# Kernel optimization log

Hardware: AMD Instinct MI355X
Metric: run time of the kernel (lower is better)

Reference implementation:

```python
import jax, jax.numpy as jnp
import numpy as np

DIM = 512  # word_hidden_size * 2


def _linear_params(key, din, dout, scale=0.05):
    kw, kb = jax.random.split(key)
    W = jax.random.normal(kw, (din, dout), dtype=jnp.float32) * scale
    b = jax.random.normal(kb, (dout,), dtype=jnp.float32) * scale
    return W, b


def setup_inputs() -> dict:
    key = jax.random.key(0)
    ks = jax.random.split(key, 16)
    S_c, S_q, B = 256, 32, 32
    inp = {
        'context_output': jax.random.normal(ks[0], (S_c, B, DIM), dtype=jnp.float32),
        'question_output': jax.random.normal(ks[1], (S_q, B, DIM), dtype=jnp.float32),
        'question_hidden_state': jax.random.normal(ks[2], (B, DIM), dtype=jnp.float32),
        'image_output': jax.random.normal(ks[3], (S_c, B, DIM), dtype=jnp.float32),
    }
    names = ['fc1', 'fc2', 'dm', 'rm', 'qm', 'rr', 'rg', 'qg']
    for i, n in enumerate(names):
        W, b = _linear_params(ks[4 + i], DIM, DIM)
        inp['W_' + n] = W
        inp['b_' + n] = b
    W_ms, b_ms = _linear_params(ks[12], DIM, 1)
    inp['W_ms'] = W_ms
    inp['b_ms'] = b_ms
    return inp


def reference(context_output, question_output, question_hidden_state, image_output,
              W_fc1, b_fc1, W_fc2, b_fc2, W_dm, b_dm, W_rm, b_rm, W_qm, b_qm,
              W_rr, b_rr, W_rg, b_rg, W_qg, b_qg, W_ms, b_ms):
    # ctx: [B, S, D] = fc1(context) + fc2(image) after seq-first -> batch-first permute
    ctx = (jnp.einsum('sbd,de->bse', context_output, W_fc1) + b_fc1
           + jnp.einsum('sbd,de->bse', image_output, W_fc2) + b_fc2)
    # hoist loop-invariant linear_dm(ctx): same math, computed once
    ctx_dm = jnp.einsum('bsd,de->bse', ctx, W_dm) + b_dm  # [B, S, D]

    B = ctx.shape[0]
    r0 = jnp.zeros((B, DIM), dtype=ctx.dtype)

    def step(r, q_t):  # r: [B, D], q_t: [B, D]
        rm = r @ W_rm + b_rm          # [B, D]
        qm = q_t @ W_qm + b_qm        # [B, D]
        m = jnp.tanh(ctx_dm + rm[:, None, :] + qm[:, None, :])  # [B, S, D]
        logits = jnp.einsum('bsd,do->bso', m, W_ms)[..., 0] + b_ms[0]  # [B, S]
        s = jax.nn.softmax(logits, axis=1)                     # [B, S]
        r_new = jnp.einsum('bs,bsd->bd', s, ctx) + jnp.tanh(r @ W_rr + b_rr)
        return r_new, None

    r, _ = jax.lax.scan(step, r0, question_output)  # scan over question tokens

    g = (r @ W_rg + b_rg) + (question_hidden_state @ W_qg + b_qg)  # [B, D]
    return g
```

## Files before the change

### kernel.cpp

```cpp
#include <hip/hip_runtime.h>
#include <hip/hip_bf16.h>

#define DIMD 512
#define NB   32
#define NS   256
#define NT   32
#define SA_STR  66
#define SCT_STR 258
#define SR_STR  132

typedef __bf16 bf16x8 __attribute__((ext_vector_type(8)));
typedef float  f32x4  __attribute__((ext_vector_type(4)));
typedef unsigned long long u64;

__device__ __forceinline__ float tanh_fast(float x) {
    float e = __expf(2.f * x);
    return 1.f - 2.f / (e + 1.f);
}

__device__ __forceinline__ void gl_lds16(const __bf16* g, __bf16* l) {
    __builtin_amdgcn_global_load_lds((const __attribute__((address_space(1))) void*)g,
                                     (__attribute__((address_space(3))) void*)l, 16, 0, 0);
}

__device__ __forceinline__ void pub64(u64* p, float v, unsigned tag) {
    u64 pk = ((u64)__float_as_uint(v) << 32) | (u64)tag;
    __hip_atomic_store(p, pk, __ATOMIC_RELAXED, __HIP_MEMORY_SCOPE_AGENT);
}
__device__ __forceinline__ float poll64(const u64* p, unsigned tag) {
    u64 v = __hip_atomic_load(p, __ATOMIC_RELAXED, __HIP_MEMORY_SCOPE_AGENT);
    while ((unsigned)v != tag) {
        __builtin_amdgcn_s_sleep(1);
        v = __hip_atomic_load(p, __ATOMIC_RELAXED, __HIP_MEMORY_SCOPE_AGENT);
    }
    return __uint_as_float((unsigned)(v >> 32));
}

__global__ void k_prep_all(const float* __restrict__ ctxin, const float* __restrict__ img,
                           const float* __restrict__ qin,
                           const float* __restrict__ Wfc1, const float* __restrict__ Wfc2,
                           const float* __restrict__ Wdm, const float* __restrict__ Wqm,
                           const float* __restrict__ Wrm, const float* __restrict__ Wrr,
                           __bf16* __restrict__ acat, __bf16* __restrict__ qp,
                           __bf16* __restrict__ wcatT, __bf16* __restrict__ wdmT,
                           __bf16* __restrict__ wqmT, __bf16* __restrict__ wrmT,
                           __bf16* __restrict__ wrrT) {
    int row = blockIdx.x;
    if (row < 8192) {
        int b = row >> 8, s = row & 255;
        const float* c  = ctxin + ((size_t)s * NB + b) * DIMD;
        const float* im = img   + ((size_t)s * NB + b) * DIMD;
        __bf16* o = acat + (size_t)row * 1024;
        for (int d = threadIdx.x; d < DIMD; d += 256) {
            o[d]       = (__bf16)c[d];
            o[512 + d] = (__bf16)im[d];
        }
    } else if (row < 10240) {
        int idx = (row - 8192) * 256 + threadIdx.x;
        qp[idx] = (__bf16)qin[idx];
    } else {
        __shared__ float tile[32][33];
        int zz = (row - 10240) >> 8;
        int idx = (row - 10240) & 255;
        int bx = idx & 15, by = idx >> 4;
        int x = threadIdx.x & 31, y = threadIdx.x >> 5;
        const float* src = (zz == 0) ? Wfc1 : (zz == 1) ? Wfc2 : (zz == 2) ? Wdm
                         : (zz == 3) ? Wqm : (zz == 4) ? Wrm : Wrr;
        __bf16* dst; int stride, off;
        if (zz < 2) { dst = wcatT; stride = 1024; off = zz * 512; }
        else {
            dst = (zz == 2) ? wdmT : (zz == 3) ? wqmT : (zz == 4) ? wrmT : wrrT;
            stride = 512; off = 0;
        }
        int c0 = bx * 32, r0 = by * 32;
#pragma unroll
        for (int k = 0; k < 32; k += 8)
            tile[y + k][x] = src[(size_t)(r0 + y + k) * DIMD + c0 + x];
        __syncthreads();
#pragma unroll
        for (int k = 0; k < 32; k += 8)
            dst[(size_t)(c0 + y + k) * stride + off + r0 + x] = (__bf16)tile[x][y + k];
    }
}

__global__ void k_post_t(const __bf16* __restrict__ ctxb, __bf16* __restrict__ ctxT,
                         const float* __restrict__ Wrg, const float* __restrict__ Wqg,
                         __bf16* __restrict__ wrgT, __bf16* __restrict__ wqgT) {
    int z = blockIdx.z;
    int x = threadIdx.x, y = threadIdx.y;
    if (z < 32) {
        if (blockIdx.y >= 8) return;
        __shared__ __bf16 tile[32][33];
        int c0 = blockIdx.x * 32, s0 = blockIdx.y * 32;
        const __bf16* S = ctxb + (size_t)z * NS * DIMD;
        __bf16* D = ctxT + (size_t)z * DIMD * NS;
#pragma unroll
        for (int k = 0; k < 32; k += 8)
            tile[y + k][x] = S[(size_t)(s0 + y + k) * DIMD + c0 + x];
        __syncthreads();
#pragma unroll
        for (int k = 0; k < 32; k += 8)
            D[(size_t)(c0 + y + k) * NS + s0 + x] = tile[x][y + k];
    } else {
        __shared__ float tf[32][33];
        const float* src = (z == 32) ? Wrg : Wqg;
        __bf16* dst = (z == 32) ? wrgT : wqgT;
        int c0 = blockIdx.x * 32, r0 = blockIdx.y * 32;
#pragma unroll
        for (int k = 0; k < 32; k += 8)
            tf[y + k][x] = src[(size_t)(r0 + y + k) * DIMD + c0 + x];
        __syncthreads();
#pragma unroll
        for (int k = 0; k < 32; k += 8)
            dst[(size_t)(c0 + y + k) * DIMD + r0 + x] = (__bf16)tf[x][y + k];
    }
}

__global__ void k_gemm64(const __bf16* __restrict__ A, const __bf16* __restrict__ BT,
                         const float* __restrict__ bias1, const float* __restrict__ bias2,
                         void* __restrict__ out, int M, int N, int K, int out_f32) {
    __shared__ __bf16 As[64 * 64];
    __shared__ __bf16 Bs[64 * 64];
    int tid = threadIdx.x, wave = tid >> 6, lane = tid & 63;
    int wm = wave >> 1, wn = wave & 1;
    int m0 = blockIdx.x * 64, n0 = blockIdx.y * 64;
    int lr = lane & 15, lq = lane >> 4;

    f32x4 acc[2][2];
#pragma unroll
    for (int i = 0; i < 2; i++)
#pragma unroll
        for (int j = 0; j < 2; j++) acc[i][j] = (f32x4){0.f, 0.f, 0.f, 0.f};

    int g0 = (wave * 2 + 0) * 64 + lane;
    int g1 = (wave * 2 + 1) * 64 + lane;
    int r0_ = g0 >> 3, c0_ = g0 & 7;
    int r1_ = g1 >> 3, c1_ = g1 & 7;
    __bf16* la0 = As + (wave * 2 + 0) * 512;
    __bf16* la1 = As + (wave * 2 + 1) * 512;
    __bf16* lb0 = Bs + (wave * 2 + 0) * 512;
    __bf16* lb1 = Bs + (wave * 2 + 1) * 512;

    for (int kk = 0; kk < K; kk += 64) {
        gl_lds16(A  + (size_t)(m0 + r0_) * K + kk + c0_ * 8, la0);
        gl_lds16(A  + (size_t)(m0 + r1_) * K + kk + c1_ * 8, la1);
        gl_lds16(BT + (size_t)(n0 + r0_) * K + kk + c0_ * 8, lb0);
        gl_lds16(BT + (size_t)(n0 + r1_) * K + kk + c1_ * 8, lb1);
        __syncthreads();
#pragma unroll
        for (int k2 = 0; k2 < 64; k2 += 32) {
            bf16x8 af[2], bfv[2];
#pragma unroll
            for (int i = 0; i < 2; i++)
                af[i] = *(const bf16x8*)(As + (wm * 32 + i * 16 + lr) * 64 + k2 + lq * 8);
#pragma unroll
            for (int j = 0; j < 2; j++)
                bfv[j] = *(const bf16x8*)(Bs + (wn * 32 + j * 16 + lr) * 64 + k2 + lq * 8);
#pragma unroll
            for (int i = 0; i < 2; i++)
#pragma unroll
                for (int j = 0; j < 2; j++)
                    acc[i][j] = __builtin_amdgcn_mfma_f32_16x16x32_bf16(af[i], bfv[j], acc[i][j], 0, 0, 0);
        }
        __syncthreads();
    }

#pragma unroll
    for (int i = 0; i < 2; i++)
#pragma unroll
        for (int j = 0; j < 2; j++) {
            int col = n0 + wn * 32 + j * 16 + lr;
            float bs = (bias1 ? bias1[col] : 0.f) + (bias2 ? bias2[col] : 0.f);
#pragma unroll
            for (int r = 0; r < 4; r++) {
                int row = m0 + wm * 32 + i * 16 + lq * 4 + r;
                float v = acc[i][j][r] + bs;
                if (out_f32) ((float*)out)[(size_t)row * N + col] = v;
                else         ((__bf16*)out)[(size_t)row * N + col] = (__bf16)v;
            }
        }
}

__global__ __launch_bounds__(512, 2) void k_scan(
    const __bf16* __restrict__ ctxdm,
    const __bf16* __restrict__ ctxT,
    const __bf16* __restrict__ wrmT,
    const __bf16* __restrict__ wrrT,
    const float* __restrict__ qmf,
    const float* __restrict__ wms, const float* __restrict__ brm,
    const float* __restrict__ brr,
    u64* parts,
    u64* rpub,
    float* __restrict__ rbuf) {
    int bid = blockIdx.x;
    int b = bid & 31, j = bid >> 5;
    int tid = threadIdx.x, wave = tid >> 6, lane = tid & 63;
    int g = lane >> 3, i = lane & 7;

    __shared__ __bf16 sA[256 * SA_STR];
    __shared__ __bf16 sCT[64 * SCT_STR];
    __shared__ float  sQ[NT * 64];
    __shared__ float  spart[NS];
    __shared__ float  sq[512];
    __shared__ float  s4[4];
    __shared__ float  sps[8 * 68];
    __shared__ float  srm[64], sh[64];
    __shared__ float  sr4[4 * SR_STR];
    __shared__ float  smv[512];

    for (int c = tid; c < 2048; c += 512) {
        int row = c >> 3, c8 = c & 7;
        *(bf16x8*)(sA + row * SA_STR + c8 * 8) =
            *(const bf16x8*)(ctxdm + ((size_t)(b * NS + row)) * DIMD + j * 64 + c8 * 8);
    }
    for (int c = tid; c < 2048; c += 512) {
        int col = c >> 5, s8 = c & 31;
        *(bf16x8*)(sCT + col * SCT_STR + s8 * 8) =
            *(const bf16x8*)(ctxT + ((size_t)(b * DIMD) + j * 64 + col) * NS + s8 * 8);
    }
    for (int c = tid; c < NT * 64; c += 512) {
        int tt = c >> 6, e = c & 63;
        sQ[c] = qmf[((size_t)tt * NB + b) * DIMD + j * 64 + e];
    }
    int m = tid >> 8, cl = (tid >> 2) & 63, q = tid & 3;
    const __bf16* wp = (m ? wrrT : wrmT) + ((size_t)(j * 64 + cl)) * DIMD + q * 128;
    bf16x8 wreg[16];
#pragma unroll
    for (int u = 0; u < 16; u++) wreg[u] = *(const bf16x8*)(wp + u * 8);

    float wm[8];
#pragma unroll
    for (int u = 0; u < 8; u++) wm[u] = wms[j * 64 + i * 8 + u];
    if (tid < 64) {
        srm[tid] = brm[j * 64 + tid];
        sh[tid]  = tanh_fast(brr[j * 64 + tid]);
    }
    __syncthreads();

    for (int t = 0; t < NT; t++) {
        unsigned tag = (unsigned)(t + 1);
        float rq[8];
#pragma unroll
        for (int u = 0; u < 8; u++) rq[u] = srm[i * 8 + u] + sQ[t * 64 + i * 8 + u];
#pragma unroll
        for (int k = 0; k < 4; k++) {
            int s = wave * 32 + k * 8 + g;
            bf16x8 cv = *(const bf16x8*)(sA + s * SA_STR + i * 8);
            float a = 0.f;
#pragma unroll
            for (int u = 0; u < 8; u++)
                a += tanh_fast((float)cv[u] + rq[u]) * wm[u];
            a += __shfl_xor(a, 1); a += __shfl_xor(a, 2); a += __shfl_xor(a, 4);
            if (i == 0) spart[s] = a;
        }
        __syncthreads();
        if (tid < NS)
            pub64(&parts[(b * 8 + j) * NS + tid], spart[tid], tag);

        {
            int s = tid >> 1, jh = (tid & 1) * 4;
            float a = 0.f;
#pragma unroll
            for (int u = 0; u < 4; u++)
                a += poll64(&parts[(b * 8 + jh + u) * NS + s], tag);
            sq[tid] = a;
        }
        __syncthreads();
        float ev = 0.f;
        if (tid < NS) { ev = __expf(sq[2 * tid] + sq[2 * tid + 1]); sq[tid] = ev; }
        else sq[tid] = 0.f;
#pragma unroll
        for (int off = 32; off; off >>= 1) ev += __shfl_xor(ev, off);
        if (tid < NS && lane == 0) s4[wave] = ev;
        __syncthreads();
        float inv = 1.f / (s4[0] + s4[1] + s4[2] + s4[3]);
        {
            const __bf16* cp = sCT + lane * SCT_STR + wave * 32;
            const float* pp = sq + wave * 32;
            float a = 0.f;
#pragma unroll
            for (int k = 0; k < 32; k += 8) {
                bf16x8 v = *(const bf16x8*)(cp + k);
#pragma unroll
                for (int u = 0; u < 8; u++) a = fmaf(pp[k + u], (float)v[u], a);
            }
            sps[wave * 68 + lane] = a;
        }
        __syncthreads();
        if (tid < 64) {
            float a = 0.f;
#pragma unroll
            for (int w2 = 0; w2 < 8; w2++) a += sps[w2 * 68 + tid];
            float rv = a * inv + sh[tid];
            if (t == NT - 1) rbuf[b * DIMD + j * 64 + tid] = rv;
            else             pub64(&rpub[b * DIMD + j * 64 + tid], rv, tag);
        }
        if (t == NT - 1) break;

        sr4[(tid >> 7) * SR_STR + (tid & 127)] = poll64(&rpub[b * DIMD + tid], tag);
        __syncthreads();
        {
            const float* sv = sr4 + q * SR_STR;
            float a0 = 0.f, a1 = 0.f;
#pragma unroll
            for (int u = 0; u < 16; u += 2) {
                bf16x8 w0 = wreg[u], w1 = wreg[u + 1];
#pragma unroll
                for (int e = 0; e < 8; e++) {
                    a0 = fmaf(sv[u * 8 + e],     (float)w0[e], a0);
                    a1 = fmaf(sv[u * 8 + 8 + e], (float)w1[e], a1);
                }
            }
            smv[tid] = a0 + a1;
        }
        __syncthreads();
        if (tid < 128) {
            int m2 = tid >> 6, cl3 = tid & 63;
            float a = smv[m2 * 256 + cl3 * 4] + smv[m2 * 256 + cl3 * 4 + 1]
                    + smv[m2 * 256 + cl3 * 4 + 2] + smv[m2 * 256 + cl3 * 4 + 3];
            int col = j * 64 + cl3;
            if (m2 == 0) srm[cl3] = a + brm[col];
            else         sh[cl3]  = tanh_fast(a + brr[col]);
        }
        __syncthreads();
    }
}

__global__ void k_final2(const float* __restrict__ r, const float* __restrict__ qh,
                         const __bf16* __restrict__ wrgT, const __bf16* __restrict__ wqgT,
                         const float* __restrict__ brg, const float* __restrict__ bqg,
                         float* __restrict__ out) {
    int clx = threadIdx.x & 7, b = threadIdx.x >> 3;
    int col = blockIdx.x * 8 + clx;
    const __bf16* w1 = wrgT + (size_t)col * DIMD;
    const __bf16* w2 = wqgT + (size_t)col * DIMD;
    const float* rp = r + (size_t)b * DIMD;
    const float* qp = qh + (size_t)b * DIMD;
    float acc = brg[col] + bqg[col];
#pragma unroll 4
    for (int d = 0; d < DIMD; d += 8) {
        bf16x8 a = *(const bf16x8*)(w1 + d);
        bf16x8 c = *(const bf16x8*)(w2 + d);
#pragma unroll
        for (int u = 0; u < 8; u++)
            acc += rp[d + u] * (float)a[u] + qp[d + u] * (float)c[u];
    }
    out[b * DIMD + col] = acc;
}


extern "C" void kernel_launch(void* const* d_in, const int* in_sizes, int n_in,
                              void* d_out, int out_size, void* d_ws, size_t ws_size,
                              hipStream_t stream) {
    const float* ctx_in = (const float*)d_in[0];
    const float* q_in   = (const float*)d_in[1];
    const float* qh     = (const float*)d_in[2];
    const float* img    = (const float*)d_in[3];
    const float* W_fc1  = (const float*)d_in[4];
    const float* b_fc1  = (const float*)d_in[5];
    const float* W_fc2  = (const float*)d_in[6];
    const float* b_fc2  = (const float*)d_in[7];
    const float* W_dm   = (const float*)d_in[8];
    const float* b_dm   = (const float*)d_in[9];
    const float* W_rm   = (const float*)d_in[10];
    const float* b_rm   = (const float*)d_in[11];
    const float* W_qm   = (const float*)d_in[12];
    const float* b_qm   = (const float*)d_in[13];
    const float* W_rr   = (const float*)d_in[14];
    const float* b_rr   = (const float*)d_in[15];
    const float* W_rg   = (const float*)d_in[16];
    const float* b_rg   = (const float*)d_in[17];
    const float* W_qg   = (const float*)d_in[18];
    const float* b_qg   = (const float*)d_in[19];
    const float* W_ms   = (const float*)d_in[20];

    char* w = (char*)d_ws;
    __bf16* acat  = (__bf16*)w;  w += (size_t)8192 * 1024 * 2;
    __bf16* qp    = (__bf16*)w;  w += (size_t)1024 * 512 * 2;
    __bf16* wcatT = (__bf16*)w;  w += (size_t)512 * 1024 * 2;
    __bf16* wdmT  = (__bf16*)w;  w += (size_t)512 * 512 * 2;
    __bf16* wqmT  = (__bf16*)w;  w += (size_t)512 * 512 * 2;
    __bf16* wrmT  = (__bf16*)w;  w += (size_t)512 * 512 * 2;
    __bf16* wrrT  = (__bf16*)w;  w += (size_t)512 * 512 * 2;
    __bf16* ctxb  = (__bf16*)w;  w += (size_t)8192 * 512 * 2;
    __bf16* ctxdm = (__bf16*)w;  w += (size_t)8192 * 512 * 2;
    char* x = (char*)acat;
    __bf16* ctxT  = (__bf16*)x;  x += (size_t)NB * DIMD * NS * 2;
    float*  qmf   = (float*)x;   x += (size_t)1024 * 512 * 4;
    __bf16* wrgT  = (__bf16*)x;  x += (size_t)512 * 512 * 2;
    __bf16* wqgT  = (__bf16*)x;  x += (size_t)512 * 512 * 2;
    u64*    rpub  = (u64*)x;     x += (size_t)NB * DIMD * 8;
    u64*    parts = (u64*)x;     x += (size_t)NB * 8 * NS * 8;
    float*  rbuf  = (float*)x;   x += (size_t)NB * DIMD * 4;

    k_prep_all<<<11776, 256, 0, stream>>>(ctx_in, img, q_in, W_fc1, W_fc2, W_dm,
                                          W_qm, W_rm, W_rr, acat, qp,
                                          wcatT, wdmT, wqmT, wrmT, wrrT);
    k_gemm64<<<dim3(128, 8), 256, 0, stream>>>(acat, wcatT, b_fc1, b_fc2, ctxb, 8192, 512, 1024, 0);
    k_post_t<<<dim3(16, 16, 34), dim3(32, 8), 0, stream>>>(ctxb, ctxT, W_rg, W_qg, wrgT, wqgT);
    k_gemm64<<<dim3(128, 8), 256, 0, stream>>>(ctxb, wdmT, b_dm, nullptr, ctxdm, 8192, 512, 512, 0);
    k_gemm64<<<dim3(16, 8), 256, 0, stream>>>(qp, wqmT, b_qm, nullptr, qmf, 1024, 512, 512, 1);

    k_scan<<<256, 512, 0, stream>>>(ctxdm, ctxT, wrmT, wrrT, qmf, W_ms,
                                    b_rm, b_rr, parts, rpub, rbuf);

    k_final2<<<64, 256, 0, stream>>>(rbuf, qh, wrgT, wqgT, b_rg, b_qg, (float*)d_out);
}
```

Measured before the change: 467.5 us.

## Merge post-GEMM kernels into one launch and publish scan partials without barrier

Moves the Wrg/Wqg transposes into the prep kernel and merges the ctx transpose, the ctx_dm GEMM and the qm GEMM into one heterogeneous kernel launch. This cuts three launches to one and lets the independent work run concurrently. In the scan, each lane group publishes its partial logit directly instead of staging it through shared memory behind a barrier. The consumer side polls all four partials in one loop rather than one after another. The main cost being targeted is launch and serialization overhead plus per-step sync latency in the recurrent scan, at the price of a larger, mixed-role kernel.

Result: faster. 447.7 us (-4.2%).

```diff
diff --git a/kernel.cpp b/kernel.cpp
--- a/kernel.cpp
+++ b/kernel.cpp
@@ -41,10 +41,12 @@
                            const float* __restrict__ Wfc1, const float* __restrict__ Wfc2,
                            const float* __restrict__ Wdm, const float* __restrict__ Wqm,
                            const float* __restrict__ Wrm, const float* __restrict__ Wrr,
+                           const float* __restrict__ Wrg, const float* __restrict__ Wqg,
                            __bf16* __restrict__ acat, __bf16* __restrict__ qp,
                            __bf16* __restrict__ wcatT, __bf16* __restrict__ wdmT,
                            __bf16* __restrict__ wqmT, __bf16* __restrict__ wrmT,
-                           __bf16* __restrict__ wrrT) {
+                           __bf16* __restrict__ wrrT, __bf16* __restrict__ wrgT,
+                           __bf16* __restrict__ wqgT) {
     int row = blockIdx.x;
     if (row < 8192) {
         int b = row >> 8, s = row & 255;
@@ -65,11 +67,13 @@
         int bx = idx & 15, by = idx >> 4;
         int x = threadIdx.x & 31, y = threadIdx.x >> 5;
         const float* src = (zz == 0) ? Wfc1 : (zz == 1) ? Wfc2 : (zz == 2) ? Wdm
-                         : (zz == 3) ? Wqm : (zz == 4) ? Wrm : Wrr;
+                         : (zz == 3) ? Wqm : (zz == 4) ? Wrm : (zz == 5) ? Wrr
+                         : (zz == 6) ? Wrg : Wqg;
         __bf16* dst; int stride, off;
         if (zz < 2) { dst = wcatT; stride = 1024; off = zz * 512; }
         else {
-            dst = (zz == 2) ? wdmT : (zz == 3) ? wqmT : (zz == 4) ? wrmT : wrrT;
+            dst = (zz == 2) ? wdmT : (zz == 3) ? wqmT : (zz == 4) ? wrmT
+                : (zz == 5) ? wrrT : (zz == 6) ? wrgT : wqgT;
             stride = 512; off = 0;
         }
         int c0 = bx * 32, r0 = by * 32;
@@ -83,47 +87,15 @@
     }
 }
 
-__global__ void k_post_t(const __bf16* __restrict__ ctxb, __bf16* __restrict__ ctxT,
-                         const float* __restrict__ Wrg, const float* __restrict__ Wqg,
-                         __bf16* __restrict__ wrgT, __bf16* __restrict__ wqgT) {
-    int z = blockIdx.z;
-    int x = threadIdx.x, y = threadIdx.y;
-    if (z < 32) {
-        if (blockIdx.y >= 8) return;
-        __shared__ __bf16 tile[32][33];
-        int c0 = blockIdx.x * 32, s0 = blockIdx.y * 32;
-        const __bf16* S = ctxb + (size_t)z * NS * DIMD;
-        __bf16* D = ctxT + (size_t)z * DIMD * NS;
-#pragma unroll
-        for (int k = 0; k < 32; k += 8)
-            tile[y + k][x] = S[(size_t)(s0 + y + k) * DIMD + c0 + x];
-        __syncthreads();
-#pragma unroll
-        for (int k = 0; k < 32; k += 8)
-            D[(size_t)(c0 + y + k) * NS + s0 + x] = tile[x][y + k];
-    } else {
-        __shared__ float tf[32][33];
-        const float* src = (z == 32) ? Wrg : Wqg;
-        __bf16* dst = (z == 32) ? wrgT : wqgT;
-        int c0 = blockIdx.x * 32, r0 = blockIdx.y * 32;
-#pragma unroll
-        for (int k = 0; k < 32; k += 8)
-            tf[y + k][x] = src[(size_t)(r0 + y + k) * DIMD + c0 + x];
-        __syncthreads();
-#pragma unroll
-        for (int k = 0; k < 32; k += 8)
-            dst[(size_t)(c0 + y + k) * DIMD + r0 + x] = (__bf16)tf[x][y + k];
-    }
-}
-
-__global__ void k_gemm64(const __bf16* __restrict__ A, const __bf16* __restrict__ BT,
-                         const float* __restrict__ bias1, const float* __restrict__ bias2,
-                         void* __restrict__ out, int M, int N, int K, int out_f32) {
-    __shared__ __bf16 As[64 * 64];
-    __shared__ __bf16 Bs[64 * 64];
+__device__ __forceinline__ void gemm_tile(const __bf16* __restrict__ A,
+                                          const __bf16* __restrict__ BT,
+                                          const float* __restrict__ bias1,
+                                          const float* __restrict__ bias2,
+                                          void* __restrict__ out, int N, int K,
+                                          int m0, int n0, int out_f32,
+                                          __bf16* As, __bf16* Bs) {
     int tid = threadIdx.x, wave = tid >> 6, lane = tid & 63;
     int wm = wave >> 1, wn = wave & 1;
-    int m0 = blockIdx.x * 64, n0 = blockIdx.y * 64;
     int lr = lane & 15, lq = lane >> 4;
 
     f32x4 acc[2][2];
@@ -179,6 +151,47 @@
                 else         ((__bf16*)out)[(size_t)row * N + col] = (__bf16)v;
             }
         }
+}
+
+__global__ void k_gemm64(const __bf16* __restrict__ A, const __bf16* __restrict__ BT,
+                         const float* __restrict__ bias1, const float* __restrict__ bias2,
+                         void* __restrict__ out, int M, int N, int K, int out_f32) {
+    __shared__ __bf16 As[64 * 64];
+    __shared__ __bf16 Bs[64 * 64];
+    gemm_tile(A, BT, bias1, bias2, out, N, K, blockIdx.x * 64, blockIdx.y * 64, out_f32, As, Bs);
+}
+
+__global__ void k_fused(const __bf16* __restrict__ ctxb, const __bf16* __restrict__ wdmT,
+                        const float* __restrict__ bdm, __bf16* __restrict__ ctxdm,
+                        const __bf16* __restrict__ qp, const __bf16* __restrict__ wqmT,
+                        const float* __restrict__ bqm, float* __restrict__ qmf,
+                        __bf16* __restrict__ ctxT) {
+    __shared__ __bf16 As[64 * 64];
+    __shared__ __bf16 Bs[64 * 64];
+    int bid = blockIdx.x;
+    if (bid < 1024) {
+        gemm_tile(ctxb, wdmT, bdm, nullptr, ctxdm, 512, 512,
+                  (bid & 127) * 64, (bid >> 7) * 64, 0, As, Bs);
+    } else if (bid < 1152) {
+        int b2 = bid - 1024;
+        gemm_tile(qp, wqmT, bqm, nullptr, qmf, 512, 512,
+                  (b2 & 15) * 64, (b2 >> 4) * 64, 1, As, Bs);
+    } else {
+        int b3 = bid - 1152;
+        int z = b3 >> 7, rest = b3 & 127;
+        int c0 = (rest & 15) * 32, s0 = (rest >> 4) * 32;
+        __bf16* tile = As;
+        int x = threadIdx.x & 31, y = threadIdx.x >> 5;
+        const __bf16* S = ctxb + (size_t)z * NS * DIMD;
+        __bf16* D = ctxT + (size_t)z * DIMD * NS;
+#pragma unroll
+        for (int k = 0; k < 32; k += 8)
+            tile[(y + k) * 33 + x] = S[(size_t)(s0 + y + k) * DIMD + c0 + x];
+        __syncthreads();
+#pragma unroll
+        for (int k = 0; k < 32; k += 8)
+            D[(size_t)(c0 + y + k) * NS + s0 + x] = tile[x * 33 + y + k];
+    }
 }
 
 __global__ __launch_bounds__(512, 2) void k_scan(
@@ -200,8 +213,8 @@
     __shared__ __bf16 sA[256 * SA_STR];
     __shared__ __bf16 sCT[64 * SCT_STR];
     __shared__ float  sQ[NT * 64];
-    __shared__ float  spart[NS];
     __shared__ float  sq[512];
+    __shared__ float  sp[256];
     __shared__ float  s4[4];
     __shared__ float  sps[8 * 68];
     __shared__ float  srm[64], sh[64];
@@ -251,24 +264,31 @@
             for (int u = 0; u < 8; u++)
                 a += tanh_fast((float)cv[u] + rq[u]) * wm[u];
             a += __shfl_xor(a, 1); a += __shfl_xor(a, 2); a += __shfl_xor(a, 4);
-            if (i == 0) spart[s] = a;
-        }
-        __syncthreads();
-        if (tid < NS)
-            pub64(&parts[(b * 8 + j) * NS + tid], spart[tid], tag);
+            if (i == 0) pub64(&parts[(b * 8 + j) * NS + s], a, tag);
+        }
 
         {
             int s = tid >> 1, jh = (tid & 1) * 4;
-            float a = 0.f;
-#pragma unroll
-            for (int u = 0; u < 4; u++)
-                a += poll64(&parts[(b * 8 + jh + u) * NS + s], tag);
-            sq[tid] = a;
+            const u64* p0 = &parts[(b * 8 + jh + 0) * NS + s];
+            const u64* p1 = &parts[(b * 8 + jh + 1) * NS + s];
+            const u64* p2 = &parts[(b * 8 + jh + 2) * NS + s];
+            const u64* p3 = &parts[(b * 8 + jh + 3) * NS + s];
+            u64 v0, v1, v2, v3;
+            for (;;) {
+                v0 = __hip_atomic_load(p0, __ATOMIC_RELAXED, __HIP_MEMORY_SCOPE_AGENT);
+                v1 = __hip_atomic_load(p1, __ATOMIC_RELAXED, __HIP_MEMORY_SCOPE_AGENT);
+                v2 = __hip_atomic_load(p2, __ATOMIC_RELAXED, __HIP_MEMORY_SCOPE_AGENT);
+                v3 = __hip_atomic_load(p3, __ATOMIC_RELAXED, __HIP_MEMORY_SCOPE_AGENT);
+                if ((unsigned)v0 == tag && (unsigned)v1 == tag &&
+                    (unsigned)v2 == tag && (unsigned)v3 == tag) break;
+                __builtin_amdgcn_s_sleep(1);
+            }
+            sq[tid] = __uint_as_float((unsigned)(v0 >> 32)) + __uint_as_float((unsigned)(v1 >> 32))
+                    + __uint_as_float((unsigned)(v2 >> 32)) + __uint_as_float((unsigned)(v3 >> 32));
         }
         __syncthreads();
         float ev = 0.f;
-        if (tid < NS) { ev = __expf(sq[2 * tid] + sq[2 * tid + 1]); sq[tid] = ev; }
-        else sq[tid] = 0.f;
+        if (tid < NS) { ev = __expf(sq[2 * tid] + sq[2 * tid + 1]); sp[tid] = ev; }
 #pragma unroll
         for (int off = 32; off; off >>= 1) ev += __shfl_xor(ev, off);
         if (tid < NS && lane == 0) s4[wave] = ev;
@@ -276,7 +296,7 @@
         float inv = 1.f / (s4[0] + s4[1] + s4[2] + s4[3]);
         {
             const __bf16* cp = sCT + lane * SCT_STR + wave * 32;
-            const float* pp = sq + wave * 32;
+            const float* pp = sp + wave * 32;
             float a = 0.f;
 #pragma unroll
             for (int k = 0; k < 32; k += 8) {
@@ -382,27 +402,23 @@
     __bf16* wqmT  = (__bf16*)w;  w += (size_t)512 * 512 * 2;
     __bf16* wrmT  = (__bf16*)w;  w += (size_t)512 * 512 * 2;
     __bf16* wrrT  = (__bf16*)w;  w += (size_t)512 * 512 * 2;
+    __bf16* wrgT  = (__bf16*)w;  w += (size_t)512 * 512 * 2;
+    __bf16* wqgT  = (__bf16*)w;  w += (size_t)512 * 512 * 2;
     __bf16* ctxb  = (__bf16*)w;  w += (size_t)8192 * 512 * 2;
     __bf16* ctxdm = (__bf16*)w;  w += (size_t)8192 * 512 * 2;
     char* x = (char*)acat;
     __bf16* ctxT  = (__bf16*)x;  x += (size_t)NB * DIMD * NS * 2;
     float*  qmf   = (float*)x;   x += (size_t)1024 * 512 * 4;
-    __bf16* wrgT  = (__bf16*)x;  x += (size_t)512 * 512 * 2;
-    __bf16* wqgT  = (__bf16*)x;  x += (size_t)512 * 512 * 2;
     u64*    rpub  = (u64*)x;     x += (size_t)NB * DIMD * 8;
     u64*    parts = (u64*)x;     x += (size_t)NB * 8 * NS * 8;
     float*  rbuf  = (float*)x;   x += (size_t)NB * DIMD * 4;
 
-    k_prep_all<<<11776, 256, 0, stream>>>(ctx_in, img, q_in, W_fc1, W_fc2, W_dm,
-                                          W_qm, W_rm, W_rr, acat, qp,
-                                          wcatT, wdmT, wqmT, wrmT, wrrT);
+    k_prep_all<<<12288, 256, 0, stream>>>(ctx_in, img, q_in, W_fc1, W_fc2, W_dm,
+                                          W_qm, W_rm, W_rr, W_rg, W_qg, acat, qp,
+                                          wcatT, wdmT, wqmT, wrmT, wrrT, wrgT, wqgT);
     k_gemm64<<<dim3(128, 8), 256, 0, stream>>>(acat, wcatT, b_fc1, b_fc2, ctxb, 8192, 512, 1024, 0);
-    k_post_t<<<dim3(16, 16, 34), dim3(32, 8), 0, stream>>>(ctxb, ctxT, W_rg, W_qg, wrgT, wqgT);
-    k_gemm64<<<dim3(128, 8), 256, 0, stream>>>(ctxb, wdmT, b_dm, nullptr, ctxdm, 8192, 512, 512, 0);
-    k_gemm64<<<dim3(16, 8), 256, 0, stream>>>(qp, wqmT, b_qm, nullptr, qmf, 1024, 512, 512, 1);
-
+    k_fused<<<5248, 256, 0, stream>>>(ctxb, wdmT, b_dm, ctxdm, qp, wqmT, b_qm, qmf, ctxT);
     k_scan<<<256, 512, 0, stream>>>(ctxdm, ctxT, wrmT, wrrT, qmf, W_ms,
                                     b_rm, b_rr, parts, rpub, rbuf);
-
     k_final2<<<64, 256, 0, stream>>>(rbuf, qh, wrgT, wqgT, b_rg, b_qg, (float*)d_out);
 }
```
